# Optimization experiments

Measured on AMD Instinct MI355X. Metric: run time of the kernel, lower is better.

The kernel has to match this reference:

```python
import jax, jax.numpy as jnp
import numpy as np

B, HW, NL = 32, 1024, 64
VD, LD, H = 1024, 768, 8
EPS = 1e-5


def _bn(x, g, b):
    # x: [B, L, C]; BatchNorm1d (train mode, batch stats) over (B, L) per channel
    m = x.mean(axis=(0, 1), keepdims=True)
    v = x.var(axis=(0, 1), keepdims=True)
    return (x - m) * jax.lax.rsqrt(v + EPS) * g + b


def _inorm(x):
    # x: [B, L, C]; InstanceNorm1d (no affine): normalize over L per (sample, channel)
    m = x.mean(axis=1, keepdims=True)
    v = x.var(axis=1, keepdims=True)
    return (x - m) * jax.lax.rsqrt(v + EPS)


def _sdpa(q_in, k_in, v_in, qw, qb, kw, kb, vw, vb, ow, ob, query_mask=None, key_mask=None):
    b, nq, d = q_in.shape
    nk = k_in.shape[1]
    dk = d // H
    q = (q_in @ qw.T + qb).reshape(b, nq, H, dk).transpose(0, 2, 1, 3)  # [b,h,nq,dk]
    k = (k_in @ kw.T + kb).reshape(b, nk, H, dk).transpose(0, 2, 1, 3)  # [b,h,nk,dk]
    v = (v_in @ vw.T + vb).reshape(b, nk, H, dk).transpose(0, 2, 1, 3)  # [b,h,nk,dk]
    if query_mask is not None:
        q = q * query_mask.reshape(b, 1, nq, 1)
    if key_mask is not None:
        k = k * key_mask.reshape(b, 1, nk, 1)
        v = v * key_mask.reshape(b, 1, nk, 1)
    att = jnp.einsum('bhqd,bhkd->bhqk', q, k) / (dk ** 0.5)
    att = jax.nn.softmax(att, axis=-1)
    out = jnp.einsum('bhqk,bhkd->bhqd', att, v)
    out = out.transpose(0, 2, 1, 3).reshape(b, nq, d)
    return out @ ow.T + ob, att


def setup_inputs() -> dict:
    key = jax.random.key(0)
    ks = iter(jax.random.split(key, 64))
    d = {
        'src': jax.random.normal(next(ks), (B, HW, VD), jnp.float32),
        'lan': jax.random.normal(next(ks), (B, NL, LD), jnp.float32),
        'pos_embed': jax.random.normal(next(ks), (B, HW, VD), jnp.float32),
        'lan_attmask': jnp.ones((B, NL), jnp.float32),
        'ip_w': jax.random.normal(next(ks), (VD, VD), jnp.float32) * 0.02,
        'ip_b': jnp.zeros((VD,), jnp.float32),
        'ip_g': jnp.ones((VD,), jnp.float32),
        'ip_beta': jnp.zeros((VD,), jnp.float32),
        'lp_w': jax.random.normal(next(ks), (VD, LD), jnp.float32) * 0.02,
        'lp_b': jnp.zeros((VD,), jnp.float32),
        'mem_tok': jax.random.normal(next(ks), (1, VD), jnp.float32) * 0.02,
        'neg_mem_tok': jax.random.normal(next(ks), (1, VD), jnp.float32) * 0.02,
    }
    for pre in ('vl', 'mf', 'ff'):
        for nm in ('q', 'k', 'v', 'o'):
            d[f'{pre}_{nm}w'] = jax.random.normal(next(ks), (VD, VD), jnp.float32) * 0.02
            d[f'{pre}_{nm}b'] = jnp.zeros((VD,), jnp.float32)
    d['op_w'] = jax.random.normal(next(ks), (VD, VD), jnp.float32) * 0.02
    d['op_b'] = jnp.zeros((VD,), jnp.float32)
    d['op_g'] = jnp.ones((VD,), jnp.float32)
    d['op_beta'] = jnp.zeros((VD,), jnp.float32)
    return d


def reference(src, lan, pos_embed, lan_attmask, ip_w, ip_b, ip_g, ip_beta, lp_w, lp_b,
              mem_tok, neg_mem_tok,
              vl_qw, vl_qb, vl_kw, vl_kb, vl_vw, vl_vb, vl_ow, vl_ob,
              mf_qw, mf_qb, mf_kw, mf_kb, mf_vw, mf_vb, mf_ow, mf_ob,
              ff_qw, ff_qb, ff_kw, ff_kb, ff_vw, ff_vb, ff_ow, ff_ob,
              op_w, op_b, op_g, op_beta):
    # input/lan projections (Conv1d k=1 == per-token linear), BN on vision path
    src_p = _bn(src @ ip_w.T + ip_b, ip_g, ip_beta)          # [B,HW,VD]
    lan_p = lan @ lp_w.T + lp_b                              # [B,NL,VD]

    # stage 1: vision-language fuse (query = language, multiplicative query mask)
    vl_out, vl_att = _sdpa(lan_p, src_p, src_p,
                           vl_qw, vl_qb, vl_kw, vl_kb, vl_vw, vl_vb, vl_ow, vl_ob,
                           query_mask=lan_attmask)
    # norms[0](vl_out) is computed in the original but its result is never used downstream

    # stage 2: memory fuse (memory tokens attend over language, key mask)
    mem_q = jnp.broadcast_to(mem_tok[None], (B, 1, VD))
    mem_out, mem_att = _sdpa(mem_q, lan_p, lan_p,
                             mf_qw, mf_qb, mf_kw, mf_kb, mf_vw, mf_vb, mf_ow, mf_ob,
                             key_mask=lan_attmask)
    neg_q = jnp.broadcast_to(neg_mem_tok[None], (B, 1, VD))
    cur = jnp.concatenate([neg_q, mem_out], axis=1)          # [B,2,VD]
    cur = _inorm(cur)                                        # norms[1], L=2>1 branch

    # stage 3: feature fuse (vision queries over memory tokens)
    ff_out, ff_att = _sdpa(src_p, cur, cur,
                           ff_qw, ff_qb, ff_kw, ff_kb, ff_vw, ff_vb, ff_ow, ff_ob)
    ff_n = _inorm(ff_out)                                    # norms[2]
    final = _bn(ff_n @ op_w.T + op_b, op_g, op_beta)         # output_proj conv + BN
    return (final, cur, vl_att, mem_att, ff_att)
```

## Files before the change

kernel.cpp:

```cpp
#include <hip/hip_runtime.h>
#include <stdint.h>

#define EPS 1e-5f
#define SCALE 0.08838834764831845f

typedef __bf16 bf16x8 __attribute__((ext_vector_type(8)));
typedef float f32x4 __attribute__((ext_vector_type(4)));
typedef unsigned short u16;
typedef unsigned int u32;
typedef u16 u16x8 __attribute__((ext_vector_type(8)));

__device__ __forceinline__ u16 f2bf(float f) {
  union { float f; u32 u; } x; x.f = f;
  u32 r = x.u + 0x7fffu + ((x.u >> 16) & 1u);
  return (u16)(r >> 16);
}
__device__ __forceinline__ float bf2f(u16 u) {
  union { u32 u; float f; } x; x.u = ((u32)u) << 16; return x.f;
}
__device__ __forceinline__ void glds16(const void* g, void* l) {
  __builtin_amdgcn_global_load_lds((__attribute__((address_space(1))) void*)g,
                                   (__attribute__((address_space(3))) void*)l,
                                   16, 0, 0);
}

struct F2B8 {
  const float* in[8];
  u16* out[8];
  int n4[8];
};
__global__ __launch_bounds__(256) void f2b_multi(F2B8 j) {
  const int seg = blockIdx.y;
  const int n4 = j.n4[seg];
  const float* __restrict__ in = j.in[seg];
  u16* __restrict__ out = j.out[seg];
  for (int i = blockIdx.x * 256 + threadIdx.x; i < n4; i += gridDim.x * 256) {
    float4 v = ((const float4*)in)[i];
    ((ushort4*)out)[i] = make_ushort4(f2bf(v.x), f2bf(v.y), f2bf(v.z), f2bf(v.w));
  }
}

struct WT2 { const float* W[2]; u16* WT[2]; };
__global__ __launch_bounds__(256)
void wtrans2(WT2 g) {
  __shared__ float tile[64][65];
  const float* __restrict__ W = g.W[blockIdx.z];
  u16* __restrict__ WT = g.WT[blockIdx.z];
  const int bx = blockIdx.x, by = blockIdx.y;
  const int r = threadIdx.x >> 2, c0 = (threadIdx.x & 3) * 16;
  const float* src = W + (size_t)(by * 64 + r) * 1024 + bx * 64 + c0;
#pragma unroll
  for (int e = 0; e < 16; e += 4) {
    float4 v = *(const float4*)(src + e);
    tile[r][c0 + e] = v.x; tile[r][c0 + e + 1] = v.y;
    tile[r][c0 + e + 2] = v.z; tile[r][c0 + e + 3] = v.w;
  }
  __syncthreads();
  u16* dst = WT + (size_t)(bx * 64 + r) * 1024 + by * 64 + c0;
#pragma unroll
  for (int e = 0; e < 16; e += 4) {
    ushort4 o = make_ushort4(f2bf(tile[c0 + e][r]), f2bf(tile[c0 + e + 1][r]),
                             f2bf(tile[c0 + e + 2][r]), f2bf(tile[c0 + e + 3][r]));
    *(ushort4*)(dst + e) = o;
  }
}

__global__ __launch_bounds__(256)
void gemm_ip(const float* __restrict__ Af, const u16* __restrict__ B,
             u16* __restrict__ Cb, float* __restrict__ ps,
             float* __restrict__ pq, int M, int N, int K) {
  __shared__ u16 sA[128 * 64];
  __shared__ u16 sB[128 * 64];
  const int nwg = (int)(gridDim.x * gridDim.y);
  const int chunk = nwg >> 3;
  int s = blockIdx.y * gridDim.x + blockIdx.x;
  int t = (s & 7) * chunk + (s >> 3);
  const int bn0 = (t & 7) * 128;
  const int bm0 = (t >> 3) * 128;
  const int tid = threadIdx.x;
  const int w = tid >> 6, l = tid & 63;
  const int wr = w >> 1, wc = w & 1;
  const int lr = l & 15, lk = l >> 4;
  const int swz = lr & 7;

  const int srow = tid >> 3;
  const int lslot = tid & 7;
  const int pslot = lslot ^ (srow & 7);
  const float* As = Af + (size_t)(bm0 + srow) * K + lslot * 8;
  const int scol = pslot << 3;
  const u16* Bb = B + (size_t)(bn0 + srow) * K + scol;
  const size_t rstride32 = (size_t)32 * K;

  f32x4 acc[4][4] = {};
  f32x4 pa0[4], pa1[4];
#pragma unroll
  for (int p = 0; p < 4; ++p) {
    const float* sp = As + (size_t)p * 32 * K;
    pa0[p] = *(const f32x4*)(sp);
    pa1[p] = *(const f32x4*)(sp + 4);
  }

  for (int k0 = 0; k0 < K; k0 += 64) {
#pragma unroll
    for (int p = 0; p < 4; ++p)
      glds16(Bb + p * rstride32 + k0, sB + p * 2048 + w * 512);
#pragma unroll
    for (int p = 0; p < 4; ++p) {
      u16x8 o;
      o[0] = f2bf(pa0[p][0]); o[1] = f2bf(pa0[p][1]);
      o[2] = f2bf(pa0[p][2]); o[3] = f2bf(pa0[p][3]);
      o[4] = f2bf(pa1[p][0]); o[5] = f2bf(pa1[p][1]);
      o[6] = f2bf(pa1[p][2]); o[7] = f2bf(pa1[p][3]);
      *(u16x8*)(sA + p * 2048 + srow * 64 + (pslot << 3)) = o;
    }
    __syncthreads();
    if (k0 + 64 < K) {
#pragma unroll
      for (int p = 0; p < 4; ++p) {
        const float* sp = As + (size_t)p * 32 * K + k0 + 64;
        pa0[p] = *(const f32x4*)(sp);
        pa1[p] = *(const f32x4*)(sp + 4);
      }
    }
#pragma unroll
    for (int ks = 0; ks < 2; ++ks) {
      const int off = (((ks << 2) + lk) ^ swz) << 3;
      bf16x8 af[4], bfr[4];
#pragma unroll
      for (int m = 0; m < 4; ++m)
        af[m] = *(const bf16x8*)(sA + (wr * 64 + m * 16 + lr) * 64 + off);
#pragma unroll
      for (int n = 0; n < 4; ++n)
        bfr[n] = *(const bf16x8*)(sB + (wc * 64 + n * 16 + lr) * 64 + off);
#pragma unroll
      for (int m = 0; m < 4; ++m)
#pragma unroll
        for (int n = 0; n < 4; ++n)
          acc[m][n] = __builtin_amdgcn_mfma_f32_16x16x32_bf16(af[m], bfr[n], acc[m][n], 0, 0, 0);
    }
    __syncthreads();
  }

#pragma unroll
  for (int m = 0; m < 4; ++m) {
    const int grow0 = bm0 + wr * 64 + m * 16 + lk * 4;
#pragma unroll
    for (int n = 0; n < 4; ++n) {
      const int gcol = bn0 + wc * 64 + n * 16 + lr;
#pragma unroll
      for (int i = 0; i < 4; ++i)
        Cb[(size_t)(grow0 + i) * N + gcol] = f2bf(acc[m][n][i]);
    }
  }

  float csum[4], csq[4];
#pragma unroll
  for (int n = 0; n < 4; ++n) {
    float s2 = 0.f, q2 = 0.f;
#pragma unroll
    for (int m = 0; m < 4; ++m)
#pragma unroll
      for (int i = 0; i < 4; ++i) {
        const float v = acc[m][n][i];
        s2 += v; q2 += v * v;
      }
    s2 += __shfl_xor(s2, 16, 64); q2 += __shfl_xor(q2, 16, 64);
    s2 += __shfl_xor(s2, 32, 64); q2 += __shfl_xor(q2, 32, 64);
    csum[n] = s2; csq[n] = q2;
  }
  float* cs = (float*)sA;
  float* cq = cs + 256;
  if (lk == 0) {
#pragma unroll
    for (int n = 0; n < 4; ++n) {
      cs[wr * 128 + wc * 64 + n * 16 + lr] = csum[n];
      cq[wr * 128 + wc * 64 + n * 16 + lr] = csq[n];
    }
  }
  __syncthreads();
  if (tid < 128) {
    const size_t o = (size_t)(bm0 >> 7) * 1024 + bn0 + tid;
    ps[o] = cs[tid] + cs[128 + tid];
    pq[o] = cq[tid] + cq[128 + tid];
  }
}

__global__ __launch_bounds__(256)
void gemm_bt(const u16* __restrict__ A, const u16* __restrict__ B,
             const float* __restrict__ bias, u16* __restrict__ Cb,
             int M, int N, int K) {
  __shared__ u16 sA[128 * 64];
  __shared__ u16 sB[128 * 64];
  const int nwg = (int)(gridDim.x * gridDim.y);
  const int chunk = nwg >> 3;
  int s = blockIdx.y * gridDim.x + blockIdx.x;
  int t = (s & 7) * chunk + (s >> 3);
  const int bn0 = (t & 7) * 128;
  const int bm0 = (t >> 3) * 128;
  const int tid = threadIdx.x;
  const int w = tid >> 6, l = tid & 63;
  const int wr = w >> 1, wc = w & 1;
  const int lr = l & 15, lk = l >> 4;
  const int swz = lr & 7;

  const int srow = tid >> 3;
  const int scol = ((tid & 7) ^ (srow & 7)) << 3;
  const u16* Ab = A + (size_t)(bm0 + srow) * K + scol;
  const u16* Bb = B + (size_t)(bn0 + srow) * K + scol;
  const size_t rstride32 = (size_t)32 * K;

  f32x4 acc[4][4] = {};

  for (int k0 = 0; k0 < K; k0 += 64) {
#pragma unroll
    for (int p = 0; p < 4; ++p) {
      glds16(Ab + p * rstride32 + k0, sA + p * 2048 + w * 512);
      glds16(Bb + p * rstride32 + k0, sB + p * 2048 + w * 512);
    }
    __syncthreads();
#pragma unroll
    for (int ks = 0; ks < 2; ++ks) {
      const int off = (((ks << 2) + lk) ^ swz) << 3;
      bf16x8 af[4], bfr[4];
#pragma unroll
      for (int m = 0; m < 4; ++m)
        af[m] = *(const bf16x8*)(sA + (wr * 64 + m * 16 + lr) * 64 + off);
#pragma unroll
      for (int n = 0; n < 4; ++n)
        bfr[n] = *(const bf16x8*)(sB + (wc * 64 + n * 16 + lr) * 64 + off);
#pragma unroll
      for (int m = 0; m < 4; ++m)
#pragma unroll
        for (int n = 0; n < 4; ++n)
          acc[m][n] = __builtin_amdgcn_mfma_f32_16x16x32_bf16(af[m], bfr[n], acc[m][n], 0, 0, 0);
    }
    __syncthreads();
  }

#pragma unroll
  for (int m = 0; m < 4; ++m) {
    const int grow0 = bm0 + wr * 64 + m * 16 + lk * 4;
#pragma unroll
    for (int n = 0; n < 4; ++n) {
      const int gcol = bn0 + wc * 64 + n * 16 + lr;
      const float bv = bias ? bias[gcol] : 0.0f;
#pragma unroll
      for (int i = 0; i < 4; ++i) {
        const float v = acc[m][n][i] + bv;
        Cb[(size_t)(grow0 + i) * N + gcol] = f2bf(v);
      }
    }
  }
}

struct G3 { const u16* B[3]; const float* bias[3]; u16* C[3]; };
__global__ __launch_bounds__(256)
void gemm_bt_z(const u16* __restrict__ A, G3 g, int M, int N, int K) {
  __shared__ u16 sA[128 * 64];
  __shared__ u16 sB[128 * 64];
  const int z = blockIdx.z;
  const u16* __restrict__ B = g.B[z];
  const float* __restrict__ bias = g.bias[z];
  u16* __restrict__ Cb = g.C[z];
  const int nwg = (int)(gridDim.x * gridDim.y);
  const int chunk = nwg >> 3;
  int s = blockIdx.y * gridDim.x + blockIdx.x;
  int t = (s & 7) * chunk + (s >> 3);
  const int bn0 = (t & 7) * 128;
  const int bm0 = (t >> 3) * 128;
  const int tid = threadIdx.x;
  const int w = tid >> 6, l = tid & 63;
  const int wr = w >> 1, wc = w & 1;
  const int lr = l & 15, lk = l >> 4;
  const int swz = lr & 7;

  const int srow = tid >> 3;
  const int scol = ((tid & 7) ^ (srow & 7)) << 3;
  const u16* Ab = A + (size_t)(bm0 + srow) * K + scol;
  const u16* Bb = B + (size_t)(bn0 + srow) * K + scol;
  const size_t rstride32 = (size_t)32 * K;

  f32x4 acc[4][4] = {};

  for (int k0 = 0; k0 < K; k0 += 64) {
#pragma unroll
    for (int p = 0; p < 4; ++p) {
      glds16(Ab + p * rstride32 + k0, sA + p * 2048 + w * 512);
      glds16(Bb + p * rstride32 + k0, sB + p * 2048 + w * 512);
    }
    __syncthreads();
#pragma unroll
    for (int ks = 0; ks < 2; ++ks) {
      const int off = (((ks << 2) + lk) ^ swz) << 3;
      bf16x8 af[4], bfr[4];
#pragma unroll
      for (int m = 0; m < 4; ++m)
        af[m] = *(const bf16x8*)(sA + (wr * 64 + m * 16 + lr) * 64 + off);
#pragma unroll
      for (int n = 0; n < 4; ++n)
        bfr[n] = *(const bf16x8*)(sB + (wc * 64 + n * 16 + lr) * 64 + off);
#pragma unroll
      for (int m = 0; m < 4; ++m)
#pragma unroll
        for (int n = 0; n < 4; ++n)
          acc[m][n] = __builtin_amdgcn_mfma_f32_16x16x32_bf16(af[m], bfr[n], acc[m][n], 0, 0, 0);
    }
    __syncthreads();
  }

#pragma unroll
  for (int m = 0; m < 4; ++m) {
    const int grow0 = bm0 + wr * 64 + m * 16 + lk * 4;
#pragma unroll
    for (int n = 0; n < 4; ++n) {
      const int gcol = bn0 + wc * 64 + n * 16 + lr;
      const float bv = bias[gcol];
#pragma unroll
      for (int i = 0; i < 4; ++i)
        Cb[(size_t)(grow0 + i) * N + gcol] = f2bf(acc[m][n][i] + bv);
    }
  }
}

__global__ __launch_bounds__(256)
void gemm_qpp(const u16* __restrict__ QV, const u16* __restrict__ WT,
              const float* __restrict__ afv, u16* __restrict__ Q2) {
  __shared__ u16 sA[128 * 64];
  __shared__ u16 sB[128 * 64];
  const int h = blockIdx.z;
  int s = blockIdx.y * 8 + blockIdx.x;
  int t = (s & 7) * 16 + (s >> 3);
  const int bn0 = (t & 7) * 128;
  const int bm0 = (t >> 3) * 128;
  const int tid = threadIdx.x;
  const int w = tid >> 6, l = tid & 63;
  const int wr = w >> 1, wc = w & 1;
  const int lr = l & 15, lk = l >> 4;
  const int swz = lr & 7;

  const int srow = tid >> 3;
  const int scol = ((tid & 7) ^ (srow & 7)) << 3;
  const u16* Ab = QV + (size_t)(bm0 + srow) * 1024 + h * 128 + scol;
  const u16* Bb = WT + (size_t)(bn0 + srow) * 1024 + h * 128 + scol;
  const size_t rstride32 = (size_t)32 * 1024;

  f32x4 acc[4][4] = {};

  for (int k0 = 0; k0 < 128; k0 += 64) {
#pragma unroll
    for (int p = 0; p < 4; ++p) {
      glds16(Ab + p * rstride32 + k0, sA + p * 2048 + w * 512);
      glds16(Bb + p * rstride32 + k0, sB + p * 2048 + w * 512);
    }
    __syncthreads();
#pragma unroll
    for (int ks = 0; ks < 2; ++ks) {
      const int off = (((ks << 2) + lk) ^ swz) << 3;
      bf16x8 af[4], bfr[4];
#pragma unroll
      for (int m = 0; m < 4; ++m)
        af[m] = *(const bf16x8*)(sA + (wr * 64 + m * 16 + lr) * 64 + off);
#pragma unroll
      for (int n = 0; n < 4; ++n)
        bfr[n] = *(const bf16x8*)(sB + (wc * 64 + n * 16 + lr) * 64 + off);
#pragma unroll
      for (int m = 0; m < 4; ++m)
#pragma unroll
        for (int n = 0; n < 4; ++n)
          acc[m][n] = __builtin_amdgcn_mfma_f32_16x16x32_bf16(af[m], bfr[n], acc[m][n], 0, 0, 0);
    }
    __syncthreads();
  }

#pragma unroll
  for (int m = 0; m < 4; ++m) {
    const int grow0 = bm0 + wr * 64 + m * 16 + lk * 4;
#pragma unroll
    for (int n = 0; n < 4; ++n) {
      const int gcol = bn0 + wc * 64 + n * 16 + lr;
      const float a = afv[gcol];
#pragma unroll
      for (int i = 0; i < 4; ++i) {
        const int gr = grow0 + i;
        const int q2row = ((gr >> 6) << 9) + h * 64 + (gr & 63);
        Q2[(size_t)q2row * 1024 + gcol] = f2bf(acc[m][n][i] * a);
      }
    }
  }
}

__global__ __launch_bounds__(512)
void vl_fused(const u16* __restrict__ Q2, const u16* __restrict__ Y1,
              const u16* __restrict__ QV, const float* __restrict__ wcv,
              const float* __restrict__ qmask, float* __restrict__ out) {
  __shared__ u16 sA[2 * 8192];
  __shared__ float redmx[64][8];
  __shared__ float redsm[64][8];
  __shared__ float cst_s[64];
  const int blk = blockIdx.x;
  const int xcd = blk & 7;
  const int idx = blk >> 3;
  const int b = xcd + 8 * (idx >> 3);
  const int r0 = (idx & 7) * 64;
  const int h = r0 >> 6;
  const int tid = threadIdx.x;
  const int w = tid >> 6, l = tid & 63;
  const int lr = l & 15, lk = l >> 4;

  const int arow0 = tid >> 4;
  const int aslot = tid & 15;
  const u16* Asrc0 = Q2 + (size_t)(b * 512 + r0 + arow0) * 1024 +
                     ((aslot ^ (arow0 & 7)) << 3);
  const u16* Asrc1 = Q2 + (size_t)(b * 512 + 32 + r0 + arow0) * 1024 +
                     ((aslot ^ ((32 + arow0) & 7)) << 3);
  const u16* Brow = Y1 + (size_t)b * 1048576 + (size_t)(w * 128 + lr) * 1024 + lk * 8;

  f32x4 acc[4][8] = {};

  glds16(Asrc0, sA + w * 512);
  glds16(Asrc1, sA + 4096 + w * 512);

  {
    const int j = tid >> 3, t8 = tid & 7;
    const u16* qp = QV + (size_t)(b * 64 + j) * 1024 + h * 128 + t8 * 16;
    const float* wp_ = wcv + h * 128 + t8 * 16;
    u16x8 v0 = *(const u16x8*)(qp);
    u16x8 v1 = *(const u16x8*)(qp + 8);
    float sacc = 0.f;
#pragma unroll
    for (int e = 0; e < 8; ++e) sacc += bf2f(v0[e]) * wp_[e];
#pragma unroll
    for (int e = 0; e < 8; ++e) sacc += bf2f(v1[e]) * wp_[8 + e];
    sacc += __shfl_xor(sacc, 1, 64);
    sacc += __shfl_xor(sacc, 2, 64);
    sacc += __shfl_xor(sacc, 4, 64);
    if (t8 == 0) cst_s[j] = sacc;
  }

  for (int c = 0; c < 8; ++c) {
    __syncthreads();
    const u16* sAc = sA + (c & 1) * 8192;
    if (c < 7) {
      const int k1 = (c + 1) * 128;
      u16* d = sA + ((c + 1) & 1) * 8192;
      glds16(Asrc0 + k1, d + w * 512);
      glds16(Asrc1 + k1, d + 4096 + w * 512);
    }
    const int k0 = c * 128;
#pragma unroll
    for (int ks = 0; ks < 4; ++ks) {
      bf16x8 af[4];
#pragma unroll
      for (int m = 0; m < 4; ++m) {
        const int row = m * 16 + lr;
        af[m] = *(const bf16x8*)(sAc + row * 128 + ((((ks << 2) + lk) ^ (lr & 7)) << 3));
      }
      const int kc = k0 + (ks << 5);
#pragma unroll
      for (int n = 0; n < 8; ++n) {
        bf16x8 bf_ = *(const bf16x8*)(Brow + (size_t)n * 16384 + kc);
#pragma unroll
        for (int m = 0; m < 4; ++m)
          acc[m][n] = __builtin_amdgcn_mfma_f32_16x16x32_bf16(af[m], bf_, acc[m][n], 0, 0, 0);
      }
    }
  }

  float cst_r[4][4], scl[4][4];
#pragma unroll
  for (int m = 0; m < 4; ++m)
#pragma unroll
    for (int i = 0; i < 4; ++i) {
      const int rl = m * 16 + lk * 4 + i;
      cst_r[m][i] = cst_s[rl];
      scl[m][i] = qmask[b * 64 + rl] * SCALE;
    }
#pragma unroll
  for (int m = 0; m < 4; ++m)
#pragma unroll
    for (int n = 0; n < 8; ++n)
#pragma unroll
      for (int i = 0; i < 4; ++i)
        acc[m][n][i] = (acc[m][n][i] + cst_r[m][i]) * scl[m][i];

  float mx[4][4];
#pragma unroll
  for (int m = 0; m < 4; ++m)
#pragma unroll
    for (int i = 0; i < 4; ++i) {
      float v = -3.4e38f;
#pragma unroll
      for (int n = 0; n < 8; ++n) v = fmaxf(v, acc[m][n][i]);
      for (int o = 1; o < 16; o <<= 1) v = fmaxf(v, __shfl_xor(v, o, 64));
      mx[m][i] = v;
    }
  if (lr == 0) {
#pragma unroll
    for (int m = 0; m < 4; ++m)
#pragma unroll
      for (int i = 0; i < 4; ++i)
        redmx[m * 16 + lk * 4 + i][w] = mx[m][i];
  }
  __syncthreads();
#pragma unroll
  for (int m = 0; m < 4; ++m)
#pragma unroll
    for (int i = 0; i < 4; ++i) {
      const int rl = m * 16 + lk * 4 + i;
      float v = redmx[rl][0];
#pragma unroll
      for (int ww = 1; ww < 8; ++ww) v = fmaxf(v, redmx[rl][ww]);
      mx[m][i] = v;
    }

  float sm[4][4];
#pragma unroll
  for (int m = 0; m < 4; ++m)
#pragma unroll
    for (int i = 0; i < 4; ++i) {
      float s = 0.f;
#pragma unroll
      for (int n = 0; n < 8; ++n) {
        float e = expf(acc[m][n][i] - mx[m][i]);
        acc[m][n][i] = e;
        s += e;
      }
      for (int o = 1; o < 16; o <<= 1) s += __shfl_xor(s, o, 64);
      sm[m][i] = s;
    }
  if (lr == 0) {
#pragma unroll
    for (int m = 0; m < 4; ++m)
#pragma unroll
      for (int i = 0; i < 4; ++i)
        redsm[m * 16 + lk * 4 + i][w] = sm[m][i];
  }
  __syncthreads();
#pragma unroll
  for (int m = 0; m < 4; ++m)
#pragma unroll
    for (int i = 0; i < 4; ++i) {
      const int rl = m * 16 + lk * 4 + i;
      float s = 0.f;
#pragma unroll
      for (int ww = 0; ww < 8; ++ww) s += redsm[rl][ww];
      sm[m][i] = 1.0f / s;
    }

#pragma unroll
  for (int m = 0; m < 4; ++m)
#pragma unroll
    for (int i = 0; i < 4; ++i) {
      const size_t grow = (size_t)(b * 512 + r0 + m * 16 + lk * 4 + i);
#pragma unroll
      for (int n = 0; n < 8; ++n)
        out[grow * 1024 + w * 128 + n * 16 + lr] = acc[m][n][i] * sm[m][i];
    }
}

__global__ __launch_bounds__(256)
void colstats_final(const float* __restrict__ ps, const float* __restrict__ pq,
                    float2* __restrict__ st, const float* __restrict__ g,
                    const float* __restrict__ be, float* __restrict__ afv,
                    float* __restrict__ cfv, float inv_n) {
  __shared__ float rs_[8][32], rq_[8][32];
  const int cg = threadIdx.x >> 5, cl = threadIdx.x & 31;
  const int col = blockIdx.x * 32 + cl;
  float s = 0.f, q = 0.f;
  for (int i = 0; i < 32; ++i) {
    const size_t idx = (size_t)(cg * 32 + i) * 1024 + col;
    s += ps[idx]; q += pq[idx];
  }
  rs_[cg][cl] = s; rq_[cg][cl] = q;
  __syncthreads();
  if (cg == 0) {
    for (int i = 1; i < 8; ++i) { s += rs_[i][cl]; q += rq_[i][cl]; }
    const float m = s * inv_n;
    const float v = q * inv_n - m * m;
    const float rs = rsqrtf(v + EPS);
    st[col] = make_float2(m, rs);
    if (afv) {
      const float a = rs * g[col];
      afv[col] = a;
      cfv[col] = be[col] - m * a;
    }
  }
}

__global__ __launch_bounds__(256)
void small_gemm(const float* __restrict__ A, const float* __restrict__ W,
                const float* __restrict__ bias, float* __restrict__ out,
                int N, int K) {
  __shared__ float sA[1024];
  const int m = blockIdx.y;
  const int n = blockIdx.x * 256 + threadIdx.x;
  for (int i = threadIdx.x; i < K; i += 256) sA[i] = A[(size_t)m * K + i];
  __syncthreads();
  const float4* w4 = (const float4*)(W + (size_t)n * K);
  const float4* a4 = (const float4*)sA;
  float acc = bias ? bias[n] : 0.0f;
  for (int k = 0; k < K / 4; ++k) {
    float4 wv = w4[k], av = a4[k];
    acc += av.x * wv.x + av.y * wv.y + av.z * wv.z + av.w * wv.w;
  }
  out[(size_t)m * N + n] = acc;
}

struct SG2 { const float* W[2]; const float* bias[2]; float* out[2]; };
__global__ __launch_bounds__(256)
void small_gemm2(const float* __restrict__ A, SG2 g, int N, int K) {
  __shared__ float sA[1024];
  const int z = blockIdx.z;
  const int m = blockIdx.y;
  const int n = blockIdx.x * 256 + threadIdx.x;
  for (int i = threadIdx.x; i < K; i += 256) sA[i] = A[(size_t)m * K + i];
  __syncthreads();
  const float4* w4 = (const float4*)(g.W[z] + (size_t)n * K);
  const float4* a4 = (const float4*)sA;
  float acc = g.bias[z][n];
  for (int k = 0; k < K / 4; ++k) {
    float4 wv = w4[k], av = a4[k];
    acc += av.x * wv.x + av.y * wv.y + av.z * wv.z + av.w * wv.w;
  }
  g.out[z][(size_t)m * N + n] = acc;
}

struct VG2 { const float* A[2]; const float* W[2]; const float* bias[2]; float* out[2]; };
__global__ __launch_bounds__(256)
void vec_gemm2(VG2 g) {
  __shared__ float sAv[1024];
  const int z = blockIdx.z;
  const float* __restrict__ A = g.A[z];
  const float* __restrict__ W = g.W[z];
  const int tid = threadIdx.x;
  ((float4*)sAv)[tid] = ((const float4*)A)[tid];
  __syncthreads();
  const int og = tid >> 3, t8 = tid & 7;
  const int n = blockIdx.x * 32 + og;
  const float* wr = W + (size_t)n * 1024;
  float s = 0.f;
#pragma unroll
  for (int j = 0; j < 32; ++j) {
    const int k = j * 32 + t8 * 4;
    float4 wv = *(const float4*)(wr + k);
    float4 av = *(const float4*)(sAv + k);
    s += av.x * wv.x + av.y * wv.y + av.z * wv.z + av.w * wv.w;
  }
  s += __shfl_xor(s, 1, 64);
  s += __shfl_xor(s, 2, 64);
  s += __shfl_xor(s, 4, 64);
  if (t8 == 0) g.out[z][n] = s + g.bias[z][n];
}

__global__ __launch_bounds__(256)
void mem_attn(const float* __restrict__ qmf, const u16* __restrict__ KM,
              const u16* __restrict__ VM, const float* __restrict__ mask,
              float* __restrict__ att_out, float* __restrict__ attv_out) {
  __shared__ float qs[1024];
  __shared__ float sS[512];
  __shared__ float sP[512];
  __shared__ float sM[64];
  const int b = blockIdx.x;
  const int tid = threadIdx.x;
  for (int i = tid; i < 1024; i += 256) qs[i] = qmf[i];
  if (tid < 64) sM[tid] = mask[b * 64 + tid];
  __syncthreads();
  for (int p = tid; p < 512; p += 256) {
    const int h = p >> 6, j = p & 63;
    const u16* kr = KM + (size_t)(b * 64 + j) * 1024 + h * 128;
    float acc = 0.f;
    for (int d = 0; d < 128; ++d) acc += qs[h * 128 + d] * bf2f(kr[d]);
    sS[p] = acc * sM[j] * SCALE;
  }
  __syncthreads();
  if (tid < 8) {
    const int h = tid;
    float mx = -3.4e38f;
    for (int j = 0; j < 64; ++j) mx = fmaxf(mx, sS[h * 64 + j]);
    float sum = 0.f;
    for (int j = 0; j < 64; ++j) {
      float e = expf(sS[h * 64 + j] - mx);
      sP[h * 64 + j] = e; sum += e;
    }
    const float inv = 1.0f / sum;
    for (int j = 0; j < 64; ++j) {
      float pp = sP[h * 64 + j] * inv;
      sP[h * 64 + j] = pp;
      att_out[(size_t)(b * 8 + h) * 64 + j] = pp;
    }
  }
  __syncthreads();
  for (int c = tid; c < 1024; c += 256) {
    const int h = c >> 7;
    float acc = 0.f;
    for (int j = 0; j < 64; ++j)
      acc += sP[h * 64 + j] * sM[j] * bf2f(VM[(size_t)(b * 64 + j) * 1024 + c]);
    attv_out[(size_t)b * 1024 + c] = acc;
  }
}

__global__ __launch_bounds__(256)
void make_cur(const float* __restrict__ neg, const float* __restrict__ memo,
              float* __restrict__ cur_out, float* __restrict__ curw) {
  const int i = blockIdx.x * 256 + threadIdx.x;
  const int b = i >> 10, c = i & 1023;
  const float a = neg[c], x = memo[i];
  const float mean = 0.5f * (a + x);
  const float d = a - mean;
  const float rs = rsqrtf(d * d + EPS);
  const float o0 = d * rs, o1 = -d * rs;
  cur_out[(size_t)(b * 2) * 1024 + c] = o0;
  cur_out[(size_t)(b * 2 + 1) * 1024 + c] = o1;
  curw[(size_t)(b * 2) * 1024 + c] = o0;
  curw[(size_t)(b * 2 + 1) * 1024 + c] = o1;
}

__global__ __launch_bounds__(256)
void ffw_fold(const float* __restrict__ kff, const float* __restrict__ wfq,
              const float* __restrict__ qb, const float* __restrict__ afv,
              const float* __restrict__ cfv, u16* __restrict__ w2ff,
              float* __restrict__ cff) {
  __shared__ float redl[4];
  const int b = blockIdx.y, jh = blockIdx.x;
  const int j = jh >> 3, h = jh & 7;
  const int tid = threadIdx.x;
  const int m0 = tid * 4;
  const float* kp = kff + (size_t)b * 2048 + j * 1024 + h * 128;
  float a0 = 0, a1 = 0, a2 = 0, a3 = 0;
  for (int n = 0; n < 128; ++n) {
    const float kv = kp[n];
    const float4 wv = *(const float4*)(wfq + (size_t)(h * 128 + n) * 1024 + m0);
    a0 += kv * wv.x; a1 += kv * wv.y; a2 += kv * wv.z; a3 += kv * wv.w;
  }
  float cpart = a0 * cfv[m0] + a1 * cfv[m0 + 1] + a2 * cfv[m0 + 2] + a3 * cfv[m0 + 3];
  if (tid < 128) cpart += qb[h * 128 + tid] * kp[tid];
  ushort4 o = make_ushort4(f2bf(a0 * afv[m0]), f2bf(a1 * afv[m0 + 1]),
                           f2bf(a2 * afv[m0 + 2]), f2bf(a3 * afv[m0 + 3]));
  *(ushort4*)(w2ff + (size_t)(b * 16 + jh) * 1024 + m0) = o;
  for (int o2 = 32; o2 > 0; o2 >>= 1) cpart += __shfl_xor(cpart, o2, 64);
  if ((tid & 63) == 0) redl[tid >> 6] = cpart;
  __syncthreads();
  if (tid == 0) cff[b * 16 + jh] = redl[0] + redl[1] + redl[2] + redl[3];
}

__global__ __launch_bounds__(256)
void ff_score(const u16* __restrict__ Y1, const u16* __restrict__ w2ff,
              const float* __restrict__ cff, float* __restrict__ P,
              float* __restrict__ att_out) {
  __shared__ u16 sB[16 * 1024];
  const int chunk = blockIdx.x, b = blockIdx.y;
  const int tid = threadIdx.x;
  const int w = tid >> 6, l = tid & 63;
  const int lr = l & 15, lk = l >> 4;
  const int swz = lr & 7;

  {
    const int n = tid >> 4;
    const int sb = (tid & 15) * 8;
#pragma unroll
    for (int v = 0; v < 8; ++v) {
      const int sidx = sb + v;
      u16x8 val = *(const u16x8*)(w2ff + (size_t)(b * 16 + n) * 1024 + sidx * 8);
      *(u16x8*)(sB + n * 1024 + ((sidx ^ (n & 7)) << 3)) = val;
    }
  }
  __syncthreads();

  const u16* Ar = Y1 + ((size_t)(b * 1024 + chunk * 128) + w * 32 + lr) * 1024 + lk * 8;
  f32x4 acc[2] = {};
#pragma unroll 4
  for (int k0 = 0; k0 < 1024; k0 += 32) {
    bf16x8 a0 = *(const bf16x8*)(Ar + k0);
    bf16x8 a1 = *(const bf16x8*)(Ar + 16 * 1024 + k0);
    const int bs = (k0 >> 3) + lk;
    bf16x8 bf_ = *(const bf16x8*)(sB + lr * 1024 + ((bs ^ swz) << 3));
    acc[0] = __builtin_amdgcn_mfma_f32_16x16x32_bf16(a0, bf_, acc[0], 0, 0, 0);
    acc[1] = __builtin_amdgcn_mfma_f32_16x16x32_bf16(a1, bf_, acc[1], 0, 0, 0);
  }

  const float cadd = cff[b * 16 + lr];
  const int h = lr & 7, jj = lr >> 3;
#pragma unroll
  for (int m = 0; m < 2; ++m)
#pragma unroll
    for (int i = 0; i < 4; ++i) {
      const float sval = (acc[m][i] + cadd) * SCALE;
      const float other = __shfl_xor(sval, 8, 64);
      const float mx = fmaxf(sval, other);
      const float e0 = expf(sval - mx), e1 = expf(other - mx);
      const float p = e0 / (e0 + e1);
      const int trow = chunk * 128 + w * 32 + m * 16 + lk * 4 + i;
      P[((size_t)b * 1024 + trow) * 16 + lr] = p;
      att_out[((size_t)(b * 8 + h) * 1024 + trow) * 2 + jj] = p;
    }
}

__global__ __launch_bounds__(256)
void pg_part(const float* __restrict__ P, float* __restrict__ Gp,
             float* __restrict__ pbarp) {
  __shared__ float Pl[128][16];
  const int b = blockIdx.x, c = blockIdx.y;
  const int tid = threadIdx.x;
  const int j = tid >> 4, j2 = tid & 15;
  for (int i = tid; i < 2048; i += 256)
    Pl[i >> 4][i & 15] = P[((size_t)b * 1024 + c * 128 + (i >> 4)) * 16 + (i & 15)];
  __syncthreads();
  float acc = 0.f, accp = 0.f;
  for (int t = 0; t < 128; ++t) {
    acc += Pl[t][j] * Pl[t][j2];
    if (j == 0) accp += Pl[t][j2];
  }
  Gp[(size_t)(b * 8 + c) * 256 + tid] = acc;
  if (j == 0) pbarp[(b * 8 + c) * 16 + j2] = accp;
}

__global__ __launch_bounds__(256)
void ufold(const float* __restrict__ vff, const u16* __restrict__ wfoT,
           float* __restrict__ U) {
  const int b = blockIdx.y, jh = blockIdx.x;
  const int j = jh >> 3, h = jh & 7;
  const int m0 = threadIdx.x * 4;
  const float* vp = vff + (size_t)b * 2048 + j * 1024 + h * 128;
  float a0 = 0, a1 = 0, a2 = 0, a3 = 0;
  for (int d = 0; d < 128; ++d) {
    const float kv = vp[d];
    ushort4 wv = *(const ushort4*)(wfoT + (size_t)(h * 128 + d) * 1024 + m0);
    a0 += kv * bf2f(wv.x); a1 += kv * bf2f(wv.y);
    a2 += kv * bf2f(wv.z); a3 += kv * bf2f(wv.w);
  }
  *(float4*)(U + (size_t)(b * 16 + jh) * 1024 + m0) = make_float4(a0, a1, a2, a3);
}

__global__ __launch_bounds__(256)
void iprep(const float* __restrict__ U, const float* __restrict__ Gp,
           const float* __restrict__ pbp, const float* __restrict__ ob,
           u16* __restrict__ U2b, float* __restrict__ G,
           float* __restrict__ pbar) {
  __shared__ float Gs[256], pb[16];
  const int b = blockIdx.x;
  const int tid = threadIdx.x;
  {
    float s = 0.f;
#pragma unroll
    for (int c = 0; c < 8; ++c) s += Gp[(size_t)(b * 8 + c) * 256 + tid];
    s *= (1.f / 1024.f);
    Gs[tid] = s;
    G[b * 256 + tid] = s;
    if (tid < 16) {
      float p = 0.f;
#pragma unroll
      for (int c = 0; c < 8; ++c) p += pbp[(b * 8 + c) * 16 + tid];
      p *= (1.f / 1024.f);
      pb[tid] = p;
      pbar[b * 16 + tid] = p;
    }
  }
  __syncthreads();
  const int m0 = tid * 4;
  float rr[4], mi4[4];
#pragma unroll
  for (int e = 0; e < 4; ++e) {
    const int m = m0 + e;
    float u[16];
#pragma unroll
    for (int jj = 0; jj < 16; ++jj) u[jj] = U[(size_t)(b * 16 + jj) * 1024 + m];
    const float o = ob[m];
    float s1 = 0.f;
#pragma unroll
    for (int jj = 0; jj < 16; ++jj) s1 += pb[jj] * u[jj];
    float q = 0.f;
#pragma unroll
    for (int jj = 0; jj < 16; ++jj) {
      float gq = 0.f;
#pragma unroll
      for (int j2 = 0; j2 < 16; ++j2) gq += Gs[jj * 16 + j2] * u[j2];
      q += u[jj] * gq;
    }
    const float mean = s1 + o;
    const float e2 = q + 2.f * o * s1 + o * o;
    const float var = fmaxf(e2 - mean * mean, 0.f);
    mi4[e] = mean;
    rr[e] = rsqrtf(var + EPS);
  }
#pragma unroll
  for (int jj = 0; jj < 16; ++jj) {
    float4 u4 = *(const float4*)(U + (size_t)(b * 16 + jj) * 1024 + m0);
    ushort4 o = make_ushort4(f2bf(u4.x * rr[0]), f2bf(u4.y * rr[1]),
                             f2bf(u4.z * rr[2]), f2bf(u4.w * rr[3]));
    *(ushort4*)(U2b + (size_t)(b * 32 + jj) * 1024 + m0) = o;
  }
  float4 ob4 = *(const float4*)(ob + m0);
  ushort4 od = make_ushort4(
      f2bf((ob4.x - mi4[0]) * rr[0]), f2bf((ob4.y - mi4[1]) * rr[1]),
      f2bf((ob4.z - mi4[2]) * rr[2]), f2bf((ob4.w - mi4[3]) * rr[3]));
  *(ushort4*)(U2b + (size_t)(b * 32 + 16) * 1024 + m0) = od;
  ushort4 z = make_ushort4(0, 0, 0, 0);
#pragma unroll
  for (int jj = 17; jj < 32; ++jj)
    *(ushort4*)(U2b + (size_t)(b * 32 + jj) * 1024 + m0) = z;
}

__global__ __launch_bounds__(256)
void w2op_gemm(const u16* __restrict__ U2b, const u16* __restrict__ wop,
               float* __restrict__ W2op) {
  __shared__ u16 sA[32 * 64];
  __shared__ u16 sB[128 * 64];
  const int b = blockIdx.y;
  const int bn0 = blockIdx.x * 128;
  const int tid = threadIdx.x;
  const int w = tid >> 6, l = tid & 63;
  const int lr = l & 15, lk = l >> 4;
  const int swz = lr & 7;
  const int srow = tid >> 3;
  const int scol = ((tid & 7) ^ (srow & 7)) << 3;
  const u16* Ab = U2b + (size_t)b * 32768 + (size_t)srow * 1024 + scol;
  const u16* Bb = wop + (size_t)(bn0 + srow) * 1024 + scol;
  const size_t rstride32 = (size_t)32 * 1024;

  f32x4 acc[2][2] = {};
  for (int k0 = 0; k0 < 1024; k0 += 64) {
    glds16(Ab + k0, sA + w * 512);
#pragma unroll
    for (int p = 0; p < 4; ++p)
      glds16(Bb + p * rstride32 + k0, sB + p * 2048 + w * 512);
    __syncthreads();
#pragma unroll
    for (int ks = 0; ks < 2; ++ks) {
      const int off = (((ks << 2) + lk) ^ swz) << 3;
      bf16x8 af[2], bfr[2];
#pragma unroll
      for (int m = 0; m < 2; ++m)
        af[m] = *(const bf16x8*)(sA + (m * 16 + lr) * 64 + off);
#pragma unroll
      for (int n = 0; n < 2; ++n)
        bfr[n] = *(const bf16x8*)(sB + (w * 32 + n * 16 + lr) * 64 + off);
#pragma unroll
      for (int m = 0; m < 2; ++m)
#pragma unroll
        for (int n = 0; n < 2; ++n)
          acc[m][n] = __builtin_amdgcn_mfma_f32_16x16x32_bf16(af[m], bfr[n], acc[m][n], 0, 0, 0);
    }
    __syncthreads();
  }
#pragma unroll
  for (int m = 0; m < 2; ++m)
#pragma unroll
    for (int n = 0; n < 2; ++n)
#pragma unroll
      for (int i = 0; i < 4; ++i) {
        const int row = m * 16 + lk * 4 + i;
        const int col = bn0 + w * 32 + n * 16 + lr;
        W2op[((size_t)b * 32 + row) * 1024 + col] = acc[m][n][i];
      }
}

__global__ __launch_bounds__(256)
void znstats_part(const float* __restrict__ W2op, const float* __restrict__ G,
                  const float* __restrict__ pbar, float* __restrict__ pmu,
                  float* __restrict__ pe2) {
  __shared__ float Gs[256], pb[16];
  const int m = blockIdx.x * 256 + threadIdx.x;
  const int bg = blockIdx.y;
  float amu = 0.f, ae2 = 0.f;
  for (int bi = 0; bi < 4; ++bi) {
    const int b = bg * 4 + bi;
    __syncthreads();
    Gs[threadIdx.x] = G[b * 256 + threadIdx.x];
    if (threadIdx.x < 16) pb[threadIdx.x] = pbar[b * 16 + threadIdx.x];
    __syncthreads();
    float wv[17];
#pragma unroll
    for (int jj = 0; jj < 17; ++jj) wv[jj] = W2op[((size_t)b * 32 + jj) * 1024 + m];
    float s1 = 0.f;
#pragma unroll
    for (int jj = 0; jj < 16; ++jj) s1 += pb[jj] * wv[jj];
    float q = 0.f;
#pragma unroll
    for (int jj = 0; jj < 16; ++jj) {
      float gq = 0.f;
#pragma unroll
      for (int j2 = 0; j2 < 16; ++j2) gq += Gs[jj * 16 + j2] * wv[j2];
      q += wv[jj] * gq;
    }
    const float cz = wv[16];
    amu += s1 + cz;
    ae2 += q + 2.f * cz * s1 + cz * cz;
  }
  pmu[bg * 1024 + m] = amu;
  pe2[bg * 1024 + m] = ae2;
}

__global__ __launch_bounds__(256)
void znfin(const float* __restrict__ pmu, const float* __restrict__ pe2,
           const float* __restrict__ g, const float* __restrict__ be,
           float* __restrict__ afin, float* __restrict__ cf0) {
  const int m = blockIdx.x * 256 + threadIdx.x;
  float mu = 0.f, e2 = 0.f;
#pragma unroll
  for (int i = 0; i < 8; ++i) { mu += pmu[i * 1024 + m]; e2 += pe2[i * 1024 + m]; }
  mu *= (1.f / 32.f); e2 *= (1.f / 32.f);
  const float var = fmaxf(e2 - mu * mu, 0.f);
  const float A = rsqrtf(var + EPS) * g[m];
  afin[m] = A;
  cf0[m] = be[m] - mu * A;
}

__global__ __launch_bounds__(256)
void zfinal(const float* __restrict__ P, const float* __restrict__ W2op,
            const float* __restrict__ afin, const float* __restrict__ cf0,
            float* __restrict__ out) {
  __shared__ float PL[512];
  const int blk = blockIdx.x;
  const int b = blk >> 5;
  const int r0 = blk * 32;
  const int tid = threadIdx.x;
  const int col = tid * 4;

  f32x4 A4 = *(const f32x4*)(afin + col);
  f32x4 wreg[17];
#pragma unroll
  for (int jj = 0; jj < 17; ++jj) {
    f32x4 wv = *(const f32x4*)(W2op + ((size_t)b * 32 + jj) * 1024 + col);
    wreg[jj] = wv * A4;
  }
  const f32x4 basev = wreg[16] + *(const f32x4*)(cf0 + col);

  if (tid < 128)
    ((f32x4*)PL)[tid] = *(const f32x4*)(P + (size_t)r0 * 16 + tid * 4);
  __syncthreads();

  float* obase = out + (size_t)r0 * 1024 + col;
  for (int r = 0; r < 32; ++r) {
    const float* pr = PL + r * 16;
    f32x4 a = basev;
#pragma unroll
    for (int jj = 0; jj < 16; ++jj) a += pr[jj] * wreg[jj];
    *(f32x4*)(obase + (size_t)r * 1024) = a;
  }
}

extern "C" void kernel_launch(void* const* d_in, const int* in_sizes, int n_in,
                              void* d_out, int out_size, void* d_ws, size_t ws_size,
                              hipStream_t stream) {
  (void)in_sizes; (void)n_in; (void)out_size; (void)ws_size;

  const float* src      = (const float*)d_in[0];
  const float* lan      = (const float*)d_in[1];
  const float* qmask    = (const float*)d_in[3];
  const float* ip_w     = (const float*)d_in[4];
  const float* ip_g     = (const float*)d_in[6];
  const float* ip_beta  = (const float*)d_in[7];
  const float* lp_w     = (const float*)d_in[8];
  const float* lp_b     = (const float*)d_in[9];
  const float* mem_tok  = (const float*)d_in[10];
  const float* neg_tok  = (const float*)d_in[11];
  const float* vl_qw    = (const float*)d_in[12];
  const float* vl_qb    = (const float*)d_in[13];
  const float* vl_kw    = (const float*)d_in[14];
  const float* vl_kb    = (const float*)d_in[15];
  const float* mf_qw    = (const float*)d_in[20];
  const float* mf_qb    = (const float*)d_in[21];
  const float* mf_kw    = (const float*)d_in[22];
  const float* mf_kb    = (const float*)d_in[23];
  const float* mf_vw    = (const float*)d_in[24];
  const float* mf_vb    = (const float*)d_in[25];
  const float* mf_ow    = (const float*)d_in[26];
  const float* mf_ob    = (const float*)d_in[27];
  const float* ff_qw    = (const float*)d_in[28];
  const float* ff_qb    = (const float*)d_in[29];
  const float* ff_kw    = (const float*)d_in[30];
  const float* ff_kb    = (const float*)d_in[31];
  const float* ff_vw    = (const float*)d_in[32];
  const float* ff_vb    = (const float*)d_in[33];
  const float* ff_ow    = (const float*)d_in[34];
  const float* ff_ob    = (const float*)d_in[35];
  const float* op_w     = (const float*)d_in[36];
  const float* op_g     = (const float*)d_in[38];
  const float* op_beta  = (const float*)d_in[39];

  float* out_final = (float*)d_out;
  float* out_cur   = out_final + 33554432ull;
  float* out_vl    = out_cur + 65536ull;
  float* out_mem   = out_vl + 16777216ull;
  float* out_ff    = out_mem + 16384ull;

  char* wp = (char*)d_ws;
  auto take = [&](size_t sz) { char* r = wp; wp += (sz + 255) & ~(size_t)255; return r; };
  u16*   W1   = (u16*)  take(67108864);
  u16*   W2   = (u16*)  take(67108864);
  u16*   LP   = (u16*)  take(4194304);
  u16*   QV   = (u16*)  take(4194304);
  u16*   KM   = (u16*)  take(4194304);
  u16*   VM   = (u16*)  take(4194304);
  u16*   LANB = (u16*)  take(3145728);
  u16*   wip  = (u16*)  take(2097152);
  u16*   wlp  = (u16*)  take(1572864);
  u16*   wvq  = (u16*)  take(2097152);
  u16*   wmk  = (u16*)  take(2097152);
  u16*   wmv  = (u16*)  take(2097152);
  u16*   wop  = (u16*)  take(2097152);
  u16*   wvkT = (u16*)  take(2097152);
  u16*   wfoT = (u16*)  take(2097152);
  u16*   w2ff = (u16*)  take(1048576);
  u16*   U2b  = (u16*)  take(2097152);
  float* qmf   = (float*)take(4096);
  float* attvm = (float*)take(131072);
  float* memo  = (float*)take(131072);
  float* curw  = (float*)take(262144);
  float* kff   = (float*)take(262144);
  float* vff   = (float*)take(262144);
  float* ps    = (float*)take(1048576);
  float* pq    = (float*)take(1048576);
  float2* st1  = (float2*)take(8192);
  float* afv   = (float*)take(4096);
  float* cfv   = (float*)take(4096);
  float* wcv   = (float*)take(4096);
  float* cff   = (float*)take(2048);
  float* Pbuf  = (float*)take(2097152);
  float* Ub    = (float*)take(2097152);
  float* W2opb = (float*)take(4194304);
  float* Gb    = (float*)take(32768);
  float* pbarb = (float*)take(2048);
  float* Gpart = (float*)take(262144);
  float* pbpart= (float*)take(16384);
  float* pmu   = (float*)take(32768);
  float* pe2   = (float*)take(32768);
  float* afin  = (float*)take(4096);
  float* cf0   = (float*)take(4096);

  const dim3 blk(256);

  {
    F2B8 j;
    const float* ins[7] = {lan, ip_w, lp_w, vl_qw, mf_kw, mf_vw, op_w};
    u16* outs[7] = {LANB, wip, wlp, wvq, wmk, wmv, wop};
    int n4s[7] = {393216, 262144, 196608, 262144, 262144, 262144, 262144};
    for (int i = 0; i < 7; ++i) { j.in[i] = ins[i]; j.out[i] = outs[i]; j.n4[i] = n4s[i]; }
    f2b_multi<<<dim3(1024, 7), blk, 0, stream>>>(j);
  }
  {
    WT2 g;
    g.W[0] = vl_kw; g.WT[0] = wvkT;
    g.W[1] = ff_ow; g.WT[1] = wfoT;
    wtrans2<<<dim3(16, 16, 2), blk, 0, stream>>>(g);
  }

  gemm_ip<<<dim3(8, 256), blk, 0, stream>>>(src, wip, W2, ps, pq, 32768, 1024, 1024);
  colstats_final<<<dim3(32), blk, 0, stream>>>(ps, pq, st1, ip_g, ip_beta, afv, cfv, 1.0f / 32768.0f);

  gemm_bt<<<dim3(8, 16), blk, 0, stream>>>(LANB, wlp, lp_b, LP, 2048, 1024, 768);
  {
    G3 g;
    g.B[0] = wvq; g.bias[0] = vl_qb; g.C[0] = QV;
    g.B[1] = wmk; g.bias[1] = mf_kb; g.C[1] = KM;
    g.B[2] = wmv; g.bias[2] = mf_vb; g.C[2] = VM;
    gemm_bt_z<<<dim3(8, 16, 3), blk, 0, stream>>>(LP, g, 2048, 1024, 1024);
  }

  gemm_qpp<<<dim3(8, 16, 8), blk, 0, stream>>>(QV, wvkT, afv, W1);
  {
    VG2 g;
    g.A[0] = cfv;     g.W[0] = vl_kw; g.bias[0] = vl_kb; g.out[0] = wcv;
    g.A[1] = mem_tok; g.W[1] = mf_qw; g.bias[1] = mf_qb; g.out[1] = qmf;
    vec_gemm2<<<dim3(32, 1, 2), blk, 0, stream>>>(g);
  }
  vl_fused<<<dim3(256), dim3(512), 0, stream>>>(W1, W2, QV, wcv, qmask, out_vl);

  mem_attn<<<dim3(32), blk, 0, stream>>>(qmf, KM, VM, qmask, out_mem, attvm);
  small_gemm<<<dim3(4, 32), blk, 0, stream>>>(attvm, mf_ow, mf_ob, memo, 1024, 1024);
  make_cur<<<dim3(128), blk, 0, stream>>>(neg_tok, memo, out_cur, curw);

  {
    SG2 g;
    g.W[0] = ff_kw; g.bias[0] = ff_kb; g.out[0] = kff;
    g.W[1] = ff_vw; g.bias[1] = ff_vb; g.out[1] = vff;
    small_gemm2<<<dim3(4, 64, 2), blk, 0, stream>>>(curw, g, 1024, 1024);
  }
  ffw_fold<<<dim3(16, 32), blk, 0, stream>>>(kff, ff_qw, ff_qb, afv, cfv, w2ff, cff);
  ff_score<<<dim3(8, 32), blk, 0, stream>>>(W2, w2ff, cff, Pbuf, out_ff);
  pg_part<<<dim3(32, 8), blk, 0, stream>>>(Pbuf, Gpart, pbpart);
  ufold<<<dim3(16, 32), blk, 0, stream>>>(vff, wfoT, Ub);
  iprep<<<dim3(32), blk, 0, stream>>>(Ub, Gpart, pbpart, ff_ob, U2b, Gb, pbarb);
  w2op_gemm<<<dim3(8, 32), blk, 0, stream>>>(U2b, wop, W2opb);
  znstats_part<<<dim3(4, 8), blk, 0, stream>>>(W2opb, Gb, pbarb, pmu, pe2);
  znfin<<<dim3(4), blk, 0, stream>>>(pmu, pe2, op_g, op_beta, afin, cf0);
  zfinal<<<dim3(1024), blk, 0, stream>>>(Pbuf, W2opb, afin, cf0, out_final);
}
```

Measured before the change: 603.0 us.

## Use bf16 weights for small GEMMs and parallelize mem_attn per head

Four more fp32 weight matrices (mf_ow, ff_qw, ff_kw, ff_vw) are added to the batched bf16 conversion kernel. The small GEMMs and ffw_fold then read bf16 weights, halving their weight traffic. mem_attn is restructured to launch one block per (batch, head) instead of per batch, using wave shuffles for the softmax and a split j-reduction. The trade-off is extra conversion work per call and reduced weight precision in those projections.

Result: faster. 545.2 us (-9.6%).

```diff
diff --git a/kernel.cpp b/kernel.cpp
--- a/kernel.cpp
+++ b/kernel.cpp
@@ -24,12 +24,12 @@
                                    16, 0, 0);
 }
 
-struct F2B8 {
-  const float* in[8];
-  u16* out[8];
-  int n4[8];
+struct F2B12 {
+  const float* in[12];
+  u16* out[12];
+  int n4[12];
 };
-__global__ __launch_bounds__(256) void f2b_multi(F2B8 j) {
+__global__ __launch_bounds__(256) void f2b_multi(F2B12 j) {
   const int seg = blockIdx.y;
   const int n4 = j.n4[seg];
   const float* __restrict__ in = j.in[seg];
@@ -588,39 +588,39 @@
 }
 
 __global__ __launch_bounds__(256)
-void small_gemm(const float* __restrict__ A, const float* __restrict__ W,
-                const float* __restrict__ bias, float* __restrict__ out,
-                int N, int K) {
+void small_gemm_bf(const float* __restrict__ A, const u16* __restrict__ Wb,
+                   const float* __restrict__ bias, float* __restrict__ out,
+                   int N, int K) {
   __shared__ float sA[1024];
   const int m = blockIdx.y;
   const int n = blockIdx.x * 256 + threadIdx.x;
   for (int i = threadIdx.x; i < K; i += 256) sA[i] = A[(size_t)m * K + i];
   __syncthreads();
-  const float4* w4 = (const float4*)(W + (size_t)n * K);
-  const float4* a4 = (const float4*)sA;
+  const u16* wr = Wb + (size_t)n * K;
   float acc = bias ? bias[n] : 0.0f;
-  for (int k = 0; k < K / 4; ++k) {
-    float4 wv = w4[k], av = a4[k];
-    acc += av.x * wv.x + av.y * wv.y + av.z * wv.z + av.w * wv.w;
+  for (int k = 0; k < K; k += 8) {
+    u16x8 wv = *(const u16x8*)(wr + k);
+#pragma unroll
+    for (int e = 0; e < 8; ++e) acc += sA[k + e] * bf2f(wv[e]);
   }
   out[(size_t)m * N + n] = acc;
 }
 
-struct SG2 { const float* W[2]; const float* bias[2]; float* out[2]; };
-__global__ __launch_bounds__(256)
-void small_gemm2(const float* __restrict__ A, SG2 g, int N, int K) {
+struct SGB2 { const u16* W[2]; const float* bias[2]; float* out[2]; };
+__global__ __launch_bounds__(256)
+void small_gemm2_bf(const float* __restrict__ A, SGB2 g, int N, int K) {
   __shared__ float sA[1024];
   const int z = blockIdx.z;
   const int m = blockIdx.y;
   const int n = blockIdx.x * 256 + threadIdx.x;
   for (int i = threadIdx.x; i < K; i += 256) sA[i] = A[(size_t)m * K + i];
   __syncthreads();
-  const float4* w4 = (const float4*)(g.W[z] + (size_t)n * K);
-  const float4* a4 = (const float4*)sA;
+  const u16* wr = g.W[z] + (size_t)n * K;
   float acc = g.bias[z][n];
-  for (int k = 0; k < K / 4; ++k) {
-    float4 wv = w4[k], av = a4[k];
-    acc += av.x * wv.x + av.y * wv.y + av.z * wv.z + av.w * wv.w;
+  for (int k = 0; k < K; k += 8) {
+    u16x8 wv = *(const u16x8*)(wr + k);
+#pragma unroll
+    for (int e = 0; e < 8; ++e) acc += sA[k + e] * bf2f(wv[e]);
   }
   g.out[z][(size_t)m * N + n] = acc;
 }
@@ -656,46 +656,51 @@
 void mem_attn(const float* __restrict__ qmf, const u16* __restrict__ KM,
               const u16* __restrict__ VM, const float* __restrict__ mask,
               float* __restrict__ att_out, float* __restrict__ attv_out) {
-  __shared__ float qs[1024];
-  __shared__ float sS[512];
-  __shared__ float sP[512];
+  __shared__ float qs[128];
   __shared__ float sM[64];
-  const int b = blockIdx.x;
+  __shared__ float sP[64];
+  __shared__ float red[128];
+  const int bh = blockIdx.x;
+  const int b = bh >> 3, h = bh & 7;
   const int tid = threadIdx.x;
-  for (int i = tid; i < 1024; i += 256) qs[i] = qmf[i];
+  if (tid < 128) qs[tid] = qmf[h * 128 + tid];
   if (tid < 64) sM[tid] = mask[b * 64 + tid];
   __syncthreads();
-  for (int p = tid; p < 512; p += 256) {
-    const int h = p >> 6, j = p & 63;
-    const u16* kr = KM + (size_t)(b * 64 + j) * 1024 + h * 128;
+  {
+    const int j = tid >> 2, q4 = tid & 3;
+    const u16* kr = KM + (size_t)(b * 64 + j) * 1024 + h * 128 + q4 * 32;
     float acc = 0.f;
-    for (int d = 0; d < 128; ++d) acc += qs[h * 128 + d] * bf2f(kr[d]);
-    sS[p] = acc * sM[j] * SCALE;
-  }
-  __syncthreads();
-  if (tid < 8) {
-    const int h = tid;
-    float mx = -3.4e38f;
-    for (int j = 0; j < 64; ++j) mx = fmaxf(mx, sS[h * 64 + j]);
-    float sum = 0.f;
-    for (int j = 0; j < 64; ++j) {
-      float e = expf(sS[h * 64 + j] - mx);
-      sP[h * 64 + j] = e; sum += e;
-    }
-    const float inv = 1.0f / sum;
-    for (int j = 0; j < 64; ++j) {
-      float pp = sP[h * 64 + j] * inv;
-      sP[h * 64 + j] = pp;
-      att_out[(size_t)(b * 8 + h) * 64 + j] = pp;
-    }
-  }
-  __syncthreads();
-  for (int c = tid; c < 1024; c += 256) {
-    const int h = c >> 7;
+#pragma unroll
+    for (int d = 0; d < 32; d += 8) {
+      u16x8 v = *(const u16x8*)(kr + d);
+#pragma unroll
+      for (int e = 0; e < 8; ++e) acc += qs[q4 * 32 + d + e] * bf2f(v[e]);
+    }
+    acc += __shfl_xor(acc, 1, 64);
+    acc += __shfl_xor(acc, 2, 64);
+    if (q4 == 0) sP[j] = acc * sM[j] * SCALE;
+  }
+  __syncthreads();
+  if (tid < 64) {
+    float s = sP[tid];
+    float mx = s;
+    for (int o = 1; o < 64; o <<= 1) mx = fmaxf(mx, __shfl_xor(mx, o, 64));
+    float e = expf(s - mx);
+    float sum = e;
+    for (int o = 1; o < 64; o <<= 1) sum += __shfl_xor(sum, o, 64);
+    float p = e / sum;
+    sP[tid] = p;
+    att_out[(size_t)(b * 8 + h) * 64 + tid] = p;
+  }
+  __syncthreads();
+  {
+    const int c = tid & 127, jg = tid >> 7;
     float acc = 0.f;
-    for (int j = 0; j < 64; ++j)
-      acc += sP[h * 64 + j] * sM[j] * bf2f(VM[(size_t)(b * 64 + j) * 1024 + c]);
-    attv_out[(size_t)b * 1024 + c] = acc;
+    for (int j = jg * 32; j < jg * 32 + 32; ++j)
+      acc += sP[j] * sM[j] * bf2f(VM[(size_t)(b * 64 + j) * 1024 + h * 128 + c]);
+    if (jg) red[c] = acc;
+    __syncthreads();
+    if (!jg) attv_out[(size_t)b * 1024 + h * 128 + c] = acc + red[c];
   }
 }
 
@@ -716,7 +721,7 @@
 }
 
 __global__ __launch_bounds__(256)
-void ffw_fold(const float* __restrict__ kff, const float* __restrict__ wfq,
+void ffw_fold(const float* __restrict__ kff, const u16* __restrict__ wfqb,
               const float* __restrict__ qb, const float* __restrict__ afv,
               const float* __restrict__ cfv, u16* __restrict__ w2ff,
               float* __restrict__ cff) {
@@ -729,8 +734,9 @@
   float a0 = 0, a1 = 0, a2 = 0, a3 = 0;
   for (int n = 0; n < 128; ++n) {
     const float kv = kp[n];
-    const float4 wv = *(const float4*)(wfq + (size_t)(h * 128 + n) * 1024 + m0);
-    a0 += kv * wv.x; a1 += kv * wv.y; a2 += kv * wv.z; a3 += kv * wv.w;
+    ushort4 wv = *(const ushort4*)(wfqb + (size_t)(h * 128 + n) * 1024 + m0);
+    a0 += kv * bf2f(wv.x); a1 += kv * bf2f(wv.y);
+    a2 += kv * bf2f(wv.z); a3 += kv * bf2f(wv.w);
   }
   float cpart = a0 * cfv[m0] + a1 * cfv[m0 + 1] + a2 * cfv[m0 + 2] + a3 * cfv[m0 + 3];
   if (tid < 128) cpart += qb[h * 128 + tid] * kp[tid];
@@ -1099,6 +1105,10 @@
   u16*   wmk  = (u16*)  take(2097152);
   u16*   wmv  = (u16*)  take(2097152);
   u16*   wop  = (u16*)  take(2097152);
+  u16*   wmo  = (u16*)  take(2097152);
+  u16*   wfqb = (u16*)  take(2097152);
+  u16*   wfk  = (u16*)  take(2097152);
+  u16*   wfv  = (u16*)  take(2097152);
   u16*   wvkT = (u16*)  take(2097152);
   u16*   wfoT = (u16*)  take(2097152);
   u16*   w2ff = (u16*)  take(1048576);
@@ -1131,12 +1141,14 @@
   const dim3 blk(256);
 
   {
-    F2B8 j;
-    const float* ins[7] = {lan, ip_w, lp_w, vl_qw, mf_kw, mf_vw, op_w};
-    u16* outs[7] = {LANB, wip, wlp, wvq, wmk, wmv, wop};
-    int n4s[7] = {393216, 262144, 196608, 262144, 262144, 262144, 262144};
-    for (int i = 0; i < 7; ++i) { j.in[i] = ins[i]; j.out[i] = outs[i]; j.n4[i] = n4s[i]; }
-    f2b_multi<<<dim3(1024, 7), blk, 0, stream>>>(j);
+    F2B12 j;
+    const float* ins[11] = {lan, ip_w, lp_w, vl_qw, mf_kw, mf_vw, op_w,
+                            mf_ow, ff_qw, ff_kw, ff_vw};
+    u16* outs[11] = {LANB, wip, wlp, wvq, wmk, wmv, wop, wmo, wfqb, wfk, wfv};
+    int n4s[11] = {393216, 262144, 196608, 262144, 262144, 262144, 262144,
+                   262144, 262144, 262144, 262144};
+    for (int i = 0; i < 11; ++i) { j.in[i] = ins[i]; j.out[i] = outs[i]; j.n4[i] = n4s[i]; }
+    f2b_multi<<<dim3(1024, 11), blk, 0, stream>>>(j);
   }
   {
     WT2 g;
@@ -1166,17 +1178,17 @@
   }
   vl_fused<<<dim3(256), dim3(512), 0, stream>>>(W1, W2, QV, wcv, qmask, out_vl);
 
-  mem_attn<<<dim3(32), blk, 0, stream>>>(qmf, KM, VM, qmask, out_mem, attvm);
-  small_gemm<<<dim3(4, 32), blk, 0, stream>>>(attvm, mf_ow, mf_ob, memo, 1024, 1024);
+  mem_attn<<<dim3(256), blk, 0, stream>>>(qmf, KM, VM, qmask, out_mem, attvm);
+  small_gemm_bf<<<dim3(4, 32), blk, 0, stream>>>(attvm, wmo, mf_ob, memo, 1024, 1024);
   make_cur<<<dim3(128), blk, 0, stream>>>(neg_tok, memo, out_cur, curw);
 
   {
-    SG2 g;
-    g.W[0] = ff_kw; g.bias[0] = ff_kb; g.out[0] = kff;
-    g.W[1] = ff_vw; g.bias[1] = ff_vb; g.out[1] = vff;
-    small_gemm2<<<dim3(4, 64, 2), blk, 0, stream>>>(curw, g, 1024, 1024);
-  }
-  ffw_fold<<<dim3(16, 32), blk, 0, stream>>>(kff, ff_qw, ff_qb, afv, cfv, w2ff, cff);
+    SGB2 g;
+    g.W[0] = wfk; g.bias[0] = ff_kb; g.out[0] = kff;
+    g.W[1] = wfv; g.bias[1] = ff_vb; g.out[1] = vff;
+    small_gemm2_bf<<<dim3(4, 64, 2), blk, 0, stream>>>(curw, g, 1024, 1024);
+  }
+  ffw_fold<<<dim3(16, 32), blk, 0, stream>>>(kff, wfqb, ff_qb, afv, cfv, w2ff, cff);
   ff_score<<<dim3(8, 32), blk, 0, stream>>>(W2, w2ff, cff, Pbuf, out_ff);
   pg_part<<<dim3(32, 8), blk, 0, stream>>>(Pbuf, Gpart, pbpart);
   ufold<<<dim3(16, 32), blk, 0, stream>>>(vff, wfoT, Ub);
```
